# Kernel optimization log

Hardware: AMD Instinct MI355X
Metric: run time of the kernel (lower is better)

The kernel has to match this reference:

```python
import jax, jax.numpy as jnp
import numpy as np

EPS = 1e-5

def group_norm(x, gamma, beta, groups):
    # x: (B, C, D, H, W)
    B, C = x.shape[0], x.shape[1]
    xr = x.reshape(B, groups, C // groups, -1)
    mean = xr.mean(axis=(2, 3), keepdims=True)
    var = xr.var(axis=(2, 3), keepdims=True)
    xn = ((xr - mean) * jax.lax.rsqrt(var + EPS)).reshape(x.shape)
    return xn * gamma[None, :, None, None, None] + beta[None, :, None, None, None]

def setup_inputs() -> dict:
    key = jax.random.key(0)
    ks = jax.random.split(key, 8)
    B, Ccls = 2, 32
    D = H = W = 64
    s = 0.05
    return {
        "x": jax.random.normal(ks[0], (B, 768, 8, 8, 8), jnp.float32),
        "out": jax.random.normal(ks[1], (B, 48, D, H, W), jnp.float32),
        "task_encoding": jax.random.normal(ks[2], (Ccls, 256, 1, 1, 1), jnp.float32),
        "gn1_g": jnp.ones((768,), jnp.float32),
        "gn1_b": jnp.zeros((768,), jnp.float32),
        "gap_w": jax.random.normal(ks[3], (256, 768), jnp.float32) * s,
        "gap_b": jnp.zeros((256,), jnp.float32),
        "ctrl_w": jax.random.normal(ks[4], (153, 512), jnp.float32) * s,
        "ctrl_b": jnp.zeros((153,), jnp.float32),
        "gn2_g": jnp.ones((48,), jnp.float32),
        "gn2_b": jnp.zeros((48,), jnp.float32),
        "pre_w": jax.random.normal(ks[5], (8, 48), jnp.float32) * s,
        "pre_b": jnp.zeros((8,), jnp.float32),
    }

def reference(x, out, task_encoding, gn1_g, gn1_b, gap_w, gap_b, ctrl_w, ctrl_b,
              gn2_g, gn2_b, pre_w, pre_b):
    B = x.shape[0]
    Ccls = task_encoding.shape[0]
    # GAP branch: GroupNorm(16,768) -> ReLU -> global avg pool -> 1x1x1 conv 768->256
    h = jax.nn.relu(group_norm(x, gn1_g, gn1_b, 16))
    pooled = h.mean(axis=(2, 3, 4))                       # (B, 768)
    x_feat = pooled @ gap_w.T + gap_b                     # (B, 256)
    # Controller: per (batch, class) params from concat(x_feat, task_encoding)
    te = task_encoding.reshape(Ccls, -1)                  # (Ccls, 256)
    params = (jnp.einsum('pf,bf->bp', ctrl_w[:, :256], x_feat)[:, None, :]
              + jnp.einsum('pf,cf->cp', ctrl_w[:, 256:], te)[None, :, :]
              + ctrl_b)                                   # (B, Ccls, 153)
    w1 = params[..., 0:64].reshape(B, Ccls, 8, 8)
    w2 = params[..., 64:128].reshape(B, Ccls, 8, 8)
    w3 = params[..., 128:136].reshape(B, Ccls, 1, 8)
    b1 = params[..., 136:144]
    b2 = params[..., 144:152]
    b3 = params[..., 152:153]
    # precls branch: GroupNorm(16,48) -> ReLU -> 1x1x1 conv 48->8
    g = jax.nn.relu(group_norm(out, gn2_g, gn2_b, 16))
    h0 = jnp.einsum('oc,bcdhw->bodhw', pre_w, g) + pre_b[None, :, None, None, None]
    # Dynamic per-class head: 8->8->8->1 pointwise MLP with ReLU between layers
    t = jax.nn.relu(jnp.einsum('bcij,bjdhw->bcidhw', w1, h0) + b1[..., None, None, None])
    t = jax.nn.relu(jnp.einsum('bcij,bcjdhw->bcidhw', w2, t) + b2[..., None, None, None])
    logits = jnp.einsum('bcij,bcjdhw->bcidhw', w3, t) + b3[..., None, None, None]
    # (B, Ccls, 1, D, H, W) -> (B, Ccls, D, H, W)
    return logits[:, :, 0]
```

## Files before the change

### kernel.cpp

```cpp
#include <hip/hip_runtime.h>

constexpr int NCLS = 32;

constexpr int WS_POOL = 64;
constexpr int WS_XF  = 1600;
constexpr int WS_PAR = 2112;
constexpr int WS_P2  = 11904;

__device__ __forceinline__ float wred(float v) {
#pragma unroll
  for (int off = 32; off > 0; off >>= 1) v += __shfl_down(v, off, 64);
  return v;
}

__device__ __forceinline__ float4 fma4(float w, float4 v, float4 a) {
  a.x = fmaf(w, v.x, a.x); a.y = fmaf(w, v.y, a.y);
  a.z = fmaf(w, v.z, a.z); a.w = fmaf(w, v.w, a.w);
  return a;
}
__device__ __forceinline__ float4 relu4(float4 a) {
  a.x = fmaxf(a.x, 0.f); a.y = fmaxf(a.y, 0.f);
  a.z = fmaxf(a.z, 0.f); a.w = fmaxf(a.w, 0.f);
  return a;
}
__device__ __forceinline__ float4 bcast4(float v) { return make_float4(v, v, v, v); }

__global__ void k1_stats(const float* __restrict__ x, const float* __restrict__ oin,
                         const float* __restrict__ g1, const float* __restrict__ b1,
                         float* __restrict__ ws) {
  int t = threadIdx.x;
  int wid = t >> 6, lane = t & 63;
  __shared__ float red[8];
  if (blockIdx.x < 768) {
    int blk = blockIdx.x;
    const float4* p = reinterpret_cast<const float4*>(oin + (size_t)blk * 32768);
    float s = 0.f, s2 = 0.f;
#pragma unroll
    for (int k = 0; k < 32; ++k) {
      float4 v = p[k * 256 + t];
      s  += v.x + v.y + v.z + v.w;
      s2 += v.x*v.x + v.y*v.y + v.z*v.z + v.w*v.w;
    }
    s = wred(s); s2 = wred(s2);
    if (lane == 0) { red[wid*2] = s; red[wid*2+1] = s2; }
    __syncthreads();
    if (t == 0) {
      ws[WS_P2 + blk*2]   = red[0]+red[2]+red[4]+red[6];
      ws[WS_P2 + blk*2+1] = red[1]+red[3]+red[5]+red[7];
    }
  } else {
    int g = blockIdx.x - 768;
    __shared__ float mstat[2];
    const float4* p = reinterpret_cast<const float4*>(x + g * 24576);
    float s = 0.f, s2 = 0.f;
#pragma unroll
    for (int k = 0; k < 24; ++k) {
      float4 v = p[k * 256 + t];
      s  += v.x + v.y + v.z + v.w;
      s2 += v.x*v.x + v.y*v.y + v.z*v.z + v.w*v.w;
    }
    s = wred(s); s2 = wred(s2);
    if (lane == 0) { red[wid*2] = s; red[wid*2+1] = s2; }
    __syncthreads();
    if (t == 0) {
      float S  = red[0]+red[2]+red[4]+red[6];
      float S2 = red[1]+red[3]+red[5]+red[7];
      float mean = S * (1.f/24576.f);
      float var  = S2 * (1.f/24576.f) - mean*mean;
      mstat[0] = mean; mstat[1] = rsqrtf(var + 1e-5f);
    }
    __syncthreads();
    float mean = mstat[0], rstd = mstat[1];
#pragma unroll
    for (int k = 0; k < 12; ++k) {
      int i = k*4 + wid;
      int c = (g & 15) * 48 + i;
      float sc = rstd * g1[c];
      float sh = b1[c] - mean * sc;
      const float* q = x + g * 24576 + i * 512;
      float acc = 0.f;
#pragma unroll
      for (int j = 0; j < 8; ++j)
        acc += fmaxf(fmaf(q[lane + j*64], sc, sh), 0.f);
      acc = wred(acc);
      if (lane == 0) ws[WS_POOL + (g >> 4) * 768 + c] = acc * (1.f/512.f);
    }
  }
}

__global__ void k2_xfeat(const float* __restrict__ gapw, const float* __restrict__ gapb,
                         float* __restrict__ ws) {
  int wid = threadIdx.x >> 6, lane = threadIdx.x & 63;
  int idx = blockIdx.x * 4 + wid;
  int b = idx >> 8, o = idx & 255;
  const float* pw = gapw + o * 768;
  const float* pp = ws + WS_POOL + b * 768;
  float s = 0.f;
#pragma unroll
  for (int i = 0; i < 12; ++i) {
    int cc = lane + i*64;
    s += pw[cc] * pp[cc];
  }
  s = wred(s);
  if (lane == 0) ws[WS_XF + idx] = s + gapb[o];
}

__global__ void k3_params(const float* __restrict__ cw, const float* __restrict__ cb,
                          const float* __restrict__ te, float* __restrict__ ws) {
  int wid = threadIdx.x >> 6, lane = threadIdx.x & 63;
  int e = blockIdx.x * 4 + wid;
  int b = e / (NCLS * 153);
  int r = e % (NCLS * 153);
  int c = r / 153, p = r % 153;
  const float* w  = cw + p * 512;
  const float* xf = ws + WS_XF + b * 256;
  const float* tv = te + c * 256;
  float s = 0.f;
#pragma unroll
  for (int i = 0; i < 4; ++i) {
    int f = lane + i*64;
    s += w[f] * xf[f] + w[256 + f] * tv[f];
  }
  s = wred(s);
  if (lane == 0) ws[WS_PAR + e] = s + cb[p];
}

__global__ __launch_bounds__(256) void k4_main(const float* __restrict__ oin,
                                               const float* __restrict__ prew,
                                               const float* __restrict__ preb,
                                               const float* __restrict__ g2,
                                               const float* __restrict__ b2,
                                               const float* __restrict__ ws,
                                               float* __restrict__ out) {
  __shared__ __align__(16) float Wl[NCLS * 160];
  __shared__ __align__(16) float prewT[384];
  __shared__ float2 ssl[48];
  __shared__ float ms[64];
  int t = threadIdx.x;
  int b = blockIdx.x >> 7, tile = blockIdx.x & 127;

  if (t < 32) {
    float S = 0.f, S2 = 0.f;
#pragma unroll
    for (int k = 0; k < 24; ++k) {
      S  += ws[WS_P2 + (t*24 + k)*2];
      S2 += ws[WS_P2 + (t*24 + k)*2 + 1];
    }
    float mean = S * (1.f/786432.f);
    float var  = S2 * (1.f/786432.f) - mean*mean;
    ms[t*2] = mean; ms[t*2+1] = rsqrtf(var + 1e-5f);
  }
  if (t < 128) {
#pragma unroll
    for (int k = 0; k < 3; ++k) {
      int i = t + k*128;
      prewT[(i % 48) * 8 + (i / 48)] = prew[i];
    }
  }
  {
    const float* wsrc = ws + WS_PAR + b * (NCLS*153);
#pragma unroll 4
    for (int cc = 0; cc < NCLS; ++cc)
      if (t < 153) Wl[cc*160 + t] = wsrc[cc*153 + t];
  }
  __syncthreads();
  if (t < 48) {
    int grp = (b << 4) + t / 3;
    float mean = ms[grp*2], rstd = ms[grp*2+1];
    float sc = rstd * g2[t];
    ssl[t] = make_float2(sc, b2[t] - mean * sc);
  }
  __syncthreads();

  const float4* ip4 = reinterpret_cast<const float4*>(oin)
                      + (size_t)b * 48 * 65536 + tile*512 + t;
  const float4* pT4 = reinterpret_cast<const float4*>(prewT);
  float4 h0a[8], h0b[8];
#pragma unroll
  for (int o = 0; o < 8; ++o) { float pb = preb[o]; h0a[o] = bcast4(pb); h0b[o] = bcast4(pb); }
#pragma unroll
  for (int c = 0; c < 48; ++c) {
    float4 va = ip4[(size_t)c * 65536];
    float4 vb = ip4[(size_t)c * 65536 + 256];
    float2 ss = ssl[c];
    float4 ga = relu4(make_float4(fmaf(va.x, ss.x, ss.y), fmaf(va.y, ss.x, ss.y),
                                  fmaf(va.z, ss.x, ss.y), fmaf(va.w, ss.x, ss.y)));
    float4 gb = relu4(make_float4(fmaf(vb.x, ss.x, ss.y), fmaf(vb.y, ss.x, ss.y),
                                  fmaf(vb.z, ss.x, ss.y), fmaf(vb.w, ss.x, ss.y)));
    float4 w0 = pT4[c*2], w1 = pT4[c*2+1];
    h0a[0] = fma4(w0.x, ga, h0a[0]); h0b[0] = fma4(w0.x, gb, h0b[0]);
    h0a[1] = fma4(w0.y, ga, h0a[1]); h0b[1] = fma4(w0.y, gb, h0b[1]);
    h0a[2] = fma4(w0.z, ga, h0a[2]); h0b[2] = fma4(w0.z, gb, h0b[2]);
    h0a[3] = fma4(w0.w, ga, h0a[3]); h0b[3] = fma4(w0.w, gb, h0b[3]);
    h0a[4] = fma4(w1.x, ga, h0a[4]); h0b[4] = fma4(w1.x, gb, h0b[4]);
    h0a[5] = fma4(w1.y, ga, h0a[5]); h0b[5] = fma4(w1.y, gb, h0b[5]);
    h0a[6] = fma4(w1.z, ga, h0a[6]); h0b[6] = fma4(w1.z, gb, h0b[6]);
    h0a[7] = fma4(w1.w, ga, h0a[7]); h0b[7] = fma4(w1.w, gb, h0b[7]);
  }

  float4* op4 = reinterpret_cast<float4*>(out)
                + (size_t)b * NCLS * 65536 + tile*512 + t;
#pragma unroll 1
  for (int cls = 0; cls < NCLS; ++cls) {
    const float4* W4 = reinterpret_cast<const float4*>(Wl + cls * 160);
    float4 b1q0 = W4[34], b1q1 = W4[35];
    float4 b2q0 = W4[36], b2q1 = W4[37];
    float4 w3q0 = W4[32], w3q1 = W4[33];
    float b3v = W4[38].x;
    float b1arr[8] = {b1q0.x,b1q0.y,b1q0.z,b1q0.w,b1q1.x,b1q1.y,b1q1.z,b1q1.w};
    float b2arr[8] = {b2q0.x,b2q0.y,b2q0.z,b2q0.w,b2q1.x,b2q1.y,b2q1.z,b2q1.w};
    float w3arr[8] = {w3q0.x,w3q0.y,w3q0.z,w3q0.w,w3q1.x,w3q1.y,w3q1.z,w3q1.w};

    float4 t1a[8], t1b[8];
#pragma unroll
    for (int i = 0; i < 8; ++i) {
      float4 w0 = W4[i*2], w1 = W4[i*2+1];
      float4 aA = bcast4(b1arr[i]), aB = bcast4(b1arr[i]);
      aA = fma4(w0.x, h0a[0], aA); aB = fma4(w0.x, h0b[0], aB);
      aA = fma4(w0.y, h0a[1], aA); aB = fma4(w0.y, h0b[1], aB);
      aA = fma4(w0.z, h0a[2], aA); aB = fma4(w0.z, h0b[2], aB);
      aA = fma4(w0.w, h0a[3], aA); aB = fma4(w0.w, h0b[3], aB);
      aA = fma4(w1.x, h0a[4], aA); aB = fma4(w1.x, h0b[4], aB);
      aA = fma4(w1.y, h0a[5], aA); aB = fma4(w1.y, h0b[5], aB);
      aA = fma4(w1.z, h0a[6], aA); aB = fma4(w1.z, h0b[6], aB);
      aA = fma4(w1.w, h0a[7], aA); aB = fma4(w1.w, h0b[7], aB);
      t1a[i] = relu4(aA); t1b[i] = relu4(aB);
    }
    float4 lgA = bcast4(b3v), lgB = bcast4(b3v);
#pragma unroll
    for (int i = 0; i < 8; ++i) {
      float4 w0 = W4[16 + i*2], w1 = W4[17 + i*2];
      float4 aA = bcast4(b2arr[i]), aB = bcast4(b2arr[i]);
      aA = fma4(w0.x, t1a[0], aA); aB = fma4(w0.x, t1b[0], aB);
      aA = fma4(w0.y, t1a[1], aA); aB = fma4(w0.y, t1b[1], aB);
      aA = fma4(w0.z, t1a[2], aA); aB = fma4(w0.z, t1b[2], aB);
      aA = fma4(w0.w, t1a[3], aA); aB = fma4(w0.w, t1b[3], aB);
      aA = fma4(w1.x, t1a[4], aA); aB = fma4(w1.x, t1b[4], aB);
      aA = fma4(w1.y, t1a[5], aA); aB = fma4(w1.y, t1b[5], aB);
      aA = fma4(w1.z, t1a[6], aA); aB = fma4(w1.z, t1b[6], aB);
      aA = fma4(w1.w, t1a[7], aA); aB = fma4(w1.w, t1b[7], aB);
      aA = relu4(aA); aB = relu4(aB);
      lgA = fma4(w3arr[i], aA, lgA); lgB = fma4(w3arr[i], aB, lgB);
    }
    op4[(size_t)cls * 65536]       = lgA;
    op4[(size_t)cls * 65536 + 256] = lgB;
  }
}

extern "C" void kernel_launch(void* const* d_in, const int* in_sizes, int n_in,
                              void* d_out, int out_size, void* d_ws, size_t ws_size,
                              hipStream_t stream) {
  const float* x    = (const float*)d_in[0];
  const float* oin  = (const float*)d_in[1];
  const float* te   = (const float*)d_in[2];
  const float* g1   = (const float*)d_in[3];
  const float* b1   = (const float*)d_in[4];
  const float* gapw = (const float*)d_in[5];
  const float* gapb = (const float*)d_in[6];
  const float* cw   = (const float*)d_in[7];
  const float* cb   = (const float*)d_in[8];
  const float* g2   = (const float*)d_in[9];
  const float* b2   = (const float*)d_in[10];
  const float* prew = (const float*)d_in[11];
  const float* preb = (const float*)d_in[12];
  float* ws  = (float*)d_ws;
  float* out = (float*)d_out;

  hipLaunchKernelGGL(k1_stats,  dim3(800),  dim3(256), 0, stream, x, oin, g1, b1, ws);
  hipLaunchKernelGGL(k2_xfeat,  dim3(128),  dim3(256), 0, stream, gapw, gapb, ws);
  hipLaunchKernelGGL(k3_params, dim3(2448), dim3(256), 0, stream, cw, cb, te, ws);
  hipLaunchKernelGGL(k4_main,   dim3(256),  dim3(256), 0, stream, oin, prew, preb, g2, b2, ws, out);
}
```

Baseline: 282.6 us.

## Split main kernel grid across class halves and single-tile pixels for more blocks

The main fused kernel now launches 1024 blocks instead of 256. Each block handles 1024 voxels (one float4 per thread) and 16 of the 32 classes, where before it handled two float4 per thread and all classes. This cuts per-thread register pressure, and launch_bounds with a minimum of 4 blocks is added so more waves fit per CU. The cost is that each h0 pre-conv (48-channel GroupNorm plus 1x1 conv) is computed twice, once per class half, so input reads and that arithmetic double.

Measured after the change: 408.1 us. 44.4% more time.

```diff
diff --git a/kernel.cpp b/kernel.cpp
--- a/kernel.cpp
+++ b/kernel.cpp
@@ -125,19 +125,22 @@
   if (lane == 0) ws[WS_PAR + e] = s + cb[p];
 }
 
-__global__ __launch_bounds__(256) void k4_main(const float* __restrict__ oin,
-                                               const float* __restrict__ prew,
-                                               const float* __restrict__ preb,
-                                               const float* __restrict__ g2,
-                                               const float* __restrict__ b2,
-                                               const float* __restrict__ ws,
-                                               float* __restrict__ out) {
-  __shared__ __align__(16) float Wl[NCLS * 160];
+__global__ __launch_bounds__(256, 4) void k4_main(const float* __restrict__ oin,
+                                                  const float* __restrict__ prew,
+                                                  const float* __restrict__ preb,
+                                                  const float* __restrict__ g2,
+                                                  const float* __restrict__ b2,
+                                                  const float* __restrict__ ws,
+                                                  float* __restrict__ out) {
+  __shared__ __align__(16) float Wl[16 * 160];
   __shared__ __align__(16) float prewT[384];
   __shared__ float2 ssl[48];
   __shared__ float ms[64];
   int t = threadIdx.x;
-  int b = blockIdx.x >> 7, tile = blockIdx.x & 127;
+  int b    = blockIdx.x >> 9;
+  int rem  = blockIdx.x & 511;
+  int tile = rem >> 1;
+  int cls0 = (rem & 1) << 4;
 
   if (t < 32) {
     float S = 0.f, S2 = 0.f;
@@ -158,9 +161,9 @@
     }
   }
   {
-    const float* wsrc = ws + WS_PAR + b * (NCLS*153);
+    const float* wsrc = ws + WS_PAR + (b * NCLS + cls0) * 153;
 #pragma unroll 4
-    for (int cc = 0; cc < NCLS; ++cc)
+    for (int cc = 0; cc < 16; ++cc)
       if (t < 153) Wl[cc*160 + t] = wsrc[cc*153 + t];
   }
   __syncthreads();
@@ -173,77 +176,68 @@
   __syncthreads();
 
   const float4* ip4 = reinterpret_cast<const float4*>(oin)
-                      + (size_t)b * 48 * 65536 + tile*512 + t;
+                      + (size_t)b * 48 * 65536 + tile*256 + t;
   const float4* pT4 = reinterpret_cast<const float4*>(prewT);
-  float4 h0a[8], h0b[8];
-#pragma unroll
-  for (int o = 0; o < 8; ++o) { float pb = preb[o]; h0a[o] = bcast4(pb); h0b[o] = bcast4(pb); }
-#pragma unroll
+  float4 h0[8];
+#pragma unroll
+  for (int o = 0; o < 8; ++o) h0[o] = bcast4(preb[o]);
+#pragma unroll 8
   for (int c = 0; c < 48; ++c) {
-    float4 va = ip4[(size_t)c * 65536];
-    float4 vb = ip4[(size_t)c * 65536 + 256];
+    float4 v = ip4[(size_t)c * 65536];
     float2 ss = ssl[c];
-    float4 ga = relu4(make_float4(fmaf(va.x, ss.x, ss.y), fmaf(va.y, ss.x, ss.y),
-                                  fmaf(va.z, ss.x, ss.y), fmaf(va.w, ss.x, ss.y)));
-    float4 gb = relu4(make_float4(fmaf(vb.x, ss.x, ss.y), fmaf(vb.y, ss.x, ss.y),
-                                  fmaf(vb.z, ss.x, ss.y), fmaf(vb.w, ss.x, ss.y)));
+    float4 g = relu4(make_float4(fmaf(v.x, ss.x, ss.y), fmaf(v.y, ss.x, ss.y),
+                                 fmaf(v.z, ss.x, ss.y), fmaf(v.w, ss.x, ss.y)));
     float4 w0 = pT4[c*2], w1 = pT4[c*2+1];
-    h0a[0] = fma4(w0.x, ga, h0a[0]); h0b[0] = fma4(w0.x, gb, h0b[0]);
-    h0a[1] = fma4(w0.y, ga, h0a[1]); h0b[1] = fma4(w0.y, gb, h0b[1]);
-    h0a[2] = fma4(w0.z, ga, h0a[2]); h0b[2] = fma4(w0.z, gb, h0b[2]);
-    h0a[3] = fma4(w0.w, ga, h0a[3]); h0b[3] = fma4(w0.w, gb, h0b[3]);
-    h0a[4] = fma4(w1.x, ga, h0a[4]); h0b[4] = fma4(w1.x, gb, h0b[4]);
-    h0a[5] = fma4(w1.y, ga, h0a[5]); h0b[5] = fma4(w1.y, gb, h0b[5]);
-    h0a[6] = fma4(w1.z, ga, h0a[6]); h0b[6] = fma4(w1.z, gb, h0b[6]);
-    h0a[7] = fma4(w1.w, ga, h0a[7]); h0b[7] = fma4(w1.w, gb, h0b[7]);
+    h0[0] = fma4(w0.x, g, h0[0]);
+    h0[1] = fma4(w0.y, g, h0[1]);
+    h0[2] = fma4(w0.z, g, h0[2]);
+    h0[3] = fma4(w0.w, g, h0[3]);
+    h0[4] = fma4(w1.x, g, h0[4]);
+    h0[5] = fma4(w1.y, g, h0[5]);
+    h0[6] = fma4(w1.z, g, h0[6]);
+    h0[7] = fma4(w1.w, g, h0[7]);
   }
 
   float4* op4 = reinterpret_cast<float4*>(out)
-                + (size_t)b * NCLS * 65536 + tile*512 + t;
+                + (size_t)(b * NCLS + cls0) * 65536 + tile*256 + t;
 #pragma unroll 1
-  for (int cls = 0; cls < NCLS; ++cls) {
-    const float4* W4 = reinterpret_cast<const float4*>(Wl + cls * 160);
-    float4 b1q0 = W4[34], b1q1 = W4[35];
-    float4 b2q0 = W4[36], b2q1 = W4[37];
-    float4 w3q0 = W4[32], w3q1 = W4[33];
-    float b3v = W4[38].x;
-    float b1arr[8] = {b1q0.x,b1q0.y,b1q0.z,b1q0.w,b1q1.x,b1q1.y,b1q1.z,b1q1.w};
-    float b2arr[8] = {b2q0.x,b2q0.y,b2q0.z,b2q0.w,b2q1.x,b2q1.y,b2q1.z,b2q1.w};
-    float w3arr[8] = {w3q0.x,w3q0.y,w3q0.z,w3q0.w,w3q1.x,w3q1.y,w3q1.z,w3q1.w};
-
-    float4 t1a[8], t1b[8];
+  for (int cls = 0; cls < 16; ++cls) {
+    const float*  Wc = Wl + cls * 160;
+    const float4* W4 = reinterpret_cast<const float4*>(Wc);
+    float4 t1[8];
 #pragma unroll
     for (int i = 0; i < 8; ++i) {
       float4 w0 = W4[i*2], w1 = W4[i*2+1];
-      float4 aA = bcast4(b1arr[i]), aB = bcast4(b1arr[i]);
-      aA = fma4(w0.x, h0a[0], aA); aB = fma4(w0.x, h0b[0], aB);
-      aA = fma4(w0.y, h0a[1], aA); aB = fma4(w0.y, h0b[1], aB);
-      aA = fma4(w0.z, h0a[2], aA); aB = fma4(w0.z, h0b[2], aB);
-      aA = fma4(w0.w, h0a[3], aA); aB = fma4(w0.w, h0b[3], aB);
-      aA = fma4(w1.x, h0a[4], aA); aB = fma4(w1.x, h0b[4], aB);
-      aA = fma4(w1.y, h0a[5], aA); aB = fma4(w1.y, h0b[5], aB);
-      aA = fma4(w1.z, h0a[6], aA); aB = fma4(w1.z, h0b[6], aB);
-      aA = fma4(w1.w, h0a[7], aA); aB = fma4(w1.w, h0b[7], aB);
-      t1a[i] = relu4(aA); t1b[i] = relu4(aB);
-    }
-    float4 lgA = bcast4(b3v), lgB = bcast4(b3v);
+      float4 a = bcast4(Wc[136 + i]);
+      a = fma4(w0.x, h0[0], a);
+      a = fma4(w0.y, h0[1], a);
+      a = fma4(w0.z, h0[2], a);
+      a = fma4(w0.w, h0[3], a);
+      a = fma4(w1.x, h0[4], a);
+      a = fma4(w1.y, h0[5], a);
+      a = fma4(w1.z, h0[6], a);
+      a = fma4(w1.w, h0[7], a);
+      t1[i] = relu4(a);
+    }
+    float4 w3q0 = W4[32], w3q1 = W4[33];
+    float w3arr[8] = {w3q0.x,w3q0.y,w3q0.z,w3q0.w,w3q1.x,w3q1.y,w3q1.z,w3q1.w};
+    float4 lg = bcast4(Wc[152]);
 #pragma unroll
     for (int i = 0; i < 8; ++i) {
       float4 w0 = W4[16 + i*2], w1 = W4[17 + i*2];
-      float4 aA = bcast4(b2arr[i]), aB = bcast4(b2arr[i]);
-      aA = fma4(w0.x, t1a[0], aA); aB = fma4(w0.x, t1b[0], aB);
-      aA = fma4(w0.y, t1a[1], aA); aB = fma4(w0.y, t1b[1], aB);
-      aA = fma4(w0.z, t1a[2], aA); aB = fma4(w0.z, t1b[2], aB);
-      aA = fma4(w0.w, t1a[3], aA); aB = fma4(w0.w, t1b[3], aB);
-      aA = fma4(w1.x, t1a[4], aA); aB = fma4(w1.x, t1b[4], aB);
-      aA = fma4(w1.y, t1a[5], aA); aB = fma4(w1.y, t1b[5], aB);
-      aA = fma4(w1.z, t1a[6], aA); aB = fma4(w1.z, t1b[6], aB);
-      aA = fma4(w1.w, t1a[7], aA); aB = fma4(w1.w, t1b[7], aB);
-      aA = relu4(aA); aB = relu4(aB);
-      lgA = fma4(w3arr[i], aA, lgA); lgB = fma4(w3arr[i], aB, lgB);
-    }
-    op4[(size_t)cls * 65536]       = lgA;
-    op4[(size_t)cls * 65536 + 256] = lgB;
+      float4 a = bcast4(Wc[144 + i]);
+      a = fma4(w0.x, t1[0], a);
+      a = fma4(w0.y, t1[1], a);
+      a = fma4(w0.z, t1[2], a);
+      a = fma4(w0.w, t1[3], a);
+      a = fma4(w1.x, t1[4], a);
+      a = fma4(w1.y, t1[5], a);
+      a = fma4(w1.z, t1[6], a);
+      a = fma4(w1.w, t1[7], a);
+      a = relu4(a);
+      lg = fma4(w3arr[i], a, lg);
+    }
+    op4[(size_t)cls * 65536] = lg;
   }
 }
 
@@ -269,5 +263,5 @@
   hipLaunchKernelGGL(k1_stats,  dim3(800),  dim3(256), 0, stream, x, oin, g1, b1, ws);
   hipLaunchKernelGGL(k2_xfeat,  dim3(128),  dim3(256), 0, stream, gapw, gapb, ws);
   hipLaunchKernelGGL(k3_params, dim3(2448), dim3(256), 0, stream, cw, cb, te, ws);
-  hipLaunchKernelGGL(k4_main,   dim3(256),  dim3(256), 0, stream, oin, prew, preb, g2, b2, ws, out);
-}
+  hipLaunchKernelGGL(k4_main,   dim3(1024), dim3(256), 0, stream, oin, prew, preb, g2, b2, ws, out);
+}
```
